# Performance work log

Measured on AMD Instinct MI355X. Metric: run time of the kernel, lower is better.

Reference implementation:

```python
import jax, jax.numpy as jnp
import numpy as np

N = 256
MAX_LENGTH = 1024
BATCH = 32768


def _transition(n):
    # HiPPO-LegS transition matrices (float64 numpy, matches torch module)
    q = np.arange(n, dtype=np.float64)
    col, row = np.meshgrid(q, q)
    r = 2 * q + 1
    M = -(np.where(row >= col, r, 0) - np.diag(q))
    T = np.sqrt(np.diag(2 * q + 1))
    A = T @ M @ np.linalg.inv(T)
    B = np.diag(T)  # squeezed (N,)
    return A, B


def _build_stacked(n, max_length):
    # Bilinear (Tustin) discretization at every timescale t=1..max_length.
    A, B = _transition(n)
    ts = np.arange(1, max_length + 1, dtype=np.float64)  # (L,)
    At = A[None] / ts[:, None, None]                     # (L,N,N)
    Bt = B[None] / ts[:, None]                           # (L,N)
    I = np.eye(n)
    lhs = I[None] - At / 2                               # (L,N,N), lower triangular
    A_stacked = np.linalg.solve(lhs, I[None] + At / 2)   # (L,N,N)
    B_stacked = np.linalg.solve(lhs, Bt[..., None])[..., 0]  # (L,N)
    return A_stacked.astype(np.float32), B_stacked.astype(np.float32)


def setup_inputs() -> dict:
    key = jax.random.key(0)
    k1, k2 = jax.random.split(key)
    A_np, B_np = _build_stacked(N, MAX_LENGTH)
    return {
        "c": jax.random.normal(k1, (BATCH, N), dtype=jnp.float32),
        "f": jax.random.normal(k2, (BATCH, 1), dtype=jnp.float32),
        "A_stacked": jnp.asarray(A_np),  # (L, N, N) buffer
        "B_stacked": jnp.asarray(B_np),  # (L, N) buffer
        "t": 512,
    }


def reference(c, f, A_stacked, B_stacked, t):
    # F.linear(c, A) == c @ A.T ; then scaled add of new value f
    A = A_stacked[t]            # (N, N)
    b = B_stacked[t]            # (N,)
    return c @ A.T + b * f      # (BATCH, N)
```

## Files before the change

### kernel.cpp

```cpp
#include <hip/hip_runtime.h>
#include <cstdint>
#include <cstddef>

typedef _Float16 half8 __attribute__((ext_vector_type(8)));
typedef float f32x4 __attribute__((ext_vector_type(4)));

static constexpr int kN  = 256;
static constexpr int kBM = 64;
static constexpr size_t kHalfB  = 64 * 1024;
static constexpr size_t kLDS    = kHalfB;

__global__ __launch_bounds__(256) void hippo_prep(
    const float* __restrict__ A_stacked, const int* __restrict__ tptr,
    _Float16* __restrict__ a16)
{
    const int t = tptr[0];
    const float* __restrict__ A = A_stacked + (size_t)t * kN * kN;
    const int tid = blockIdx.x * 256 + threadIdx.x;
    const int ksh = tid >> 12;
    const int nt  = (tid >> 8) & 15;
    const int ks2 = (tid >> 6) & 3;
    const int l   = tid & 63;
    const int row = nt * 16 + (l & 15);
    const int k0  = (ksh * 4 + ks2) * 32 + ((l >> 4) << 3);
    const float* __restrict__ src = A + (size_t)row * kN + k0;
    f32x4 v0 = *(const f32x4*)(src);
    f32x4 v1 = *(const f32x4*)(src + 4);
    half8 h;
    h[0] = (_Float16)v0[0]; h[1] = (_Float16)v0[1];
    h[2] = (_Float16)v0[2]; h[3] = (_Float16)v0[3];
    h[4] = (_Float16)v1[0]; h[5] = (_Float16)v1[1];
    h[6] = (_Float16)v1[2]; h[7] = (_Float16)v1[3];
    ((half8*)a16)[tid] = h;
}

__global__ __launch_bounds__(256, 2) void hippo_gemm(
    const float* __restrict__ c, const float* __restrict__ f,
    const float* __restrict__ Bst, const int* __restrict__ tptr,
    const _Float16* __restrict__ a16, float* __restrict__ out)
{
    extern __shared__ char lds_raw[];

    const int tid  = threadIdx.x;
    const int l    = tid & 63;
    const int wid  = tid >> 6;
    const int lo16 = l & 15;
    const int hi4  = l >> 4;
    const int bid  = blockIdx.x;
    const int m0   = bid * kBM + wid * 16;

    const char* __restrict__ gsrc1 = (const char*)a16 + kHalfB;
    #pragma unroll
    for (int j = 0; j < 4; ++j) {
        const int nt = wid + j * 4;
        const int kmax = (nt - 8) >> 1;
        for (int ks2 = 0; ks2 <= kmax && ks2 < 4; ++ks2) {
            const size_t off = (size_t)(nt * 4 + ks2) * 1024 + (size_t)l * 16;
            __builtin_amdgcn_global_load_lds(
                (const __attribute__((address_space(1))) void*)(gsrc1 + off),
                (__attribute__((address_space(3))) void*)(lds_raw + off),
                16, 0, 0);
        }
    }

    const float* __restrict__ cptr = c + (size_t)(m0 + lo16) * kN + (hi4 << 3);
    f32x4 cv0[4], cv1[4];
    #pragma unroll
    for (int ks = 0; ks < 4; ++ks) {
        cv0[ks] = *(const f32x4*)(cptr + 128 + ks * 32);
        cv1[ks] = *(const f32x4*)(cptr + 128 + ks * 32 + 4);
    }

    const int t = tptr[0];
    const float* __restrict__ brow = Bst + (size_t)t * kN;
    float bvs[16];
    #pragma unroll
    for (int nt = 0; nt < 16; ++nt) bvs[nt] = brow[nt * 16 + lo16];
    float fv[4];
    #pragma unroll
    for (int r = 0; r < 4; ++r) fv[r] = f[m0 + (hi4 << 2) + r];

    __syncthreads();

    half8 af[4];
    #pragma unroll
    for (int ks = 0; ks < 4; ++ks) {
        af[ks][0] = (_Float16)cv0[ks][0]; af[ks][1] = (_Float16)cv0[ks][1];
        af[ks][2] = (_Float16)cv0[ks][2]; af[ks][3] = (_Float16)cv0[ks][3];
        af[ks][4] = (_Float16)cv1[ks][0]; af[ks][5] = (_Float16)cv1[ks][1];
        af[ks][6] = (_Float16)cv1[ks][2]; af[ks][7] = (_Float16)cv1[ks][3];
    }

    f32x4 dv0[4], dv1[4];
    #pragma unroll
    for (int ks = 0; ks < 4; ++ks) {
        dv0[ks] = *(const f32x4*)(cptr + ks * 32);
        dv1[ks] = *(const f32x4*)(cptr + ks * 32 + 4);
    }

    const half8* __restrict__ Bs = (const half8*)lds_raw;
    f32x4 acc[16];
    #pragma unroll
    for (int i = 0; i < 16; ++i) acc[i] = (f32x4){0.f, 0.f, 0.f, 0.f};
    #pragma unroll
    for (int ks2 = 0; ks2 < 4; ++ks2) {
        #pragma unroll
        for (int nt = 0; nt < 16; ++nt) {
            if (nt >= 8 + 2 * ks2) {
                half8 bf = Bs[(nt * 4 + ks2) * 64 + l];
                acc[nt] = __builtin_amdgcn_mfma_f32_16x16x32_f16(af[ks2], bf, acc[nt], 0, 0, 0);
            }
        }
    }

    __syncthreads();

    const char* __restrict__ gsrc0 = (const char*)a16;
    #pragma unroll
    for (int j = 0; j < 4; ++j) {
        const int nt = wid + j * 4;
        const int kmax = nt >> 1;
        for (int ks2 = 0; ks2 <= kmax && ks2 < 4; ++ks2) {
            const size_t off = (size_t)(nt * 4 + ks2) * 1024 + (size_t)l * 16;
            __builtin_amdgcn_global_load_lds(
                (const __attribute__((address_space(1))) void*)(gsrc0 + off),
                (__attribute__((address_space(3))) void*)(lds_raw + off),
                16, 0, 0);
        }
    }
    half8 ag[4];
    #pragma unroll
    for (int ks = 0; ks < 4; ++ks) {
        ag[ks][0] = (_Float16)dv0[ks][0]; ag[ks][1] = (_Float16)dv0[ks][1];
        ag[ks][2] = (_Float16)dv0[ks][2]; ag[ks][3] = (_Float16)dv0[ks][3];
        ag[ks][4] = (_Float16)dv1[ks][0]; ag[ks][5] = (_Float16)dv1[ks][1];
        ag[ks][6] = (_Float16)dv1[ks][2]; ag[ks][7] = (_Float16)dv1[ks][3];
    }

    __syncthreads();

    float* __restrict__ obase = out + (size_t)(m0 + (hi4 << 2)) * kN + lo16;
    #pragma unroll
    for (int nt = 0; nt < 16; ++nt) {
        f32x4 a = acc[nt];
        #pragma unroll
        for (int ks2 = 0; ks2 < 4; ++ks2) {
            if (ks2 <= (nt >> 1)) {
                half8 bf = Bs[(nt * 4 + ks2) * 64 + l];
                a = __builtin_amdgcn_mfma_f32_16x16x32_f16(ag[ks2], bf, a, 0, 0, 0);
            }
        }
        #pragma unroll
        for (int r = 0; r < 4; ++r)
            obase[(size_t)r * kN + nt * 16] = a[r] + bvs[nt] * fv[r];
    }
}

extern "C" void kernel_launch(void* const* d_in, const int* in_sizes, int n_in,
                              void* d_out, int out_size, void* d_ws, size_t ws_size,
                              hipStream_t stream) {
    const float* c   = (const float*)d_in[0];
    const float* f   = (const float*)d_in[1];
    const float* A   = (const float*)d_in[2];
    const float* B   = (const float*)d_in[3];
    const int*   t   = (const int*)d_in[4];
    float* out = (float*)d_out;
    _Float16* a16 = (_Float16*)d_ws;

    const int batch = in_sizes[0] / kN;

    hipFuncSetAttribute((const void*)hippo_gemm,
                        hipFuncAttributeMaxDynamicSharedMemorySize,
                        (int)kLDS);

    hipLaunchKernelGGL(hippo_prep, dim3(32), dim3(256), 0, stream, A, t, a16);
    hipLaunchKernelGGL(hippo_gemm, dim3(batch / kBM), dim3(256), kLDS, stream,
                       c, f, B, t, a16, out);
}
```

Measured before the change: 22.08 us.

## Pack triangular A fragments into one LDS buffer and load once

Replaces the two-phase LDS staging of the fp16 A matrix (upper-k half, compute, sync, reload lower-k half, sync) with a single packed triangular layout. Only the nonzero fragments of the lower-triangular A are stored, addressed through a prefix-offset table, so everything fits in 72 KB of LDS. This removes two barriers and the reload stall between the halves. The cost is more LDS per block, which may lower occupancy below the two blocks per CU the launch bounds request, plus constant-memory table lookups in the address math.

Result: no change. 22.44 us (+1.6%).

```diff
diff --git a/kernel.cpp b/kernel.cpp
--- a/kernel.cpp
+++ b/kernel.cpp
@@ -7,8 +7,10 @@
 
 static constexpr int kN  = 256;
 static constexpr int kBM = 64;
-static constexpr size_t kHalfB  = 64 * 1024;
-static constexpr size_t kLDS    = kHalfB;
+static constexpr size_t kLDS = 72 * 1024;
+
+__device__ __constant__ const int kBase[16] =
+    {0, 1, 2, 4, 6, 9, 12, 16, 20, 25, 30, 36, 42, 49, 56, 64};
 
 __global__ __launch_bounds__(256) void hippo_prep(
     const float* __restrict__ A_stacked, const int* __restrict__ tptr,
@@ -49,17 +51,22 @@
     const int bid  = blockIdx.x;
     const int m0   = bid * kBM + wid * 16;
 
-    const char* __restrict__ gsrc1 = (const char*)a16 + kHalfB;
+    const char* __restrict__ gsrc = (const char*)a16;
     #pragma unroll
     for (int j = 0; j < 4; ++j) {
-        const int nt = wid + j * 4;
-        const int kmax = (nt - 8) >> 1;
-        for (int ks2 = 0; ks2 <= kmax && ks2 < 4; ++ks2) {
-            const size_t off = (size_t)(nt * 4 + ks2) * 1024 + (size_t)l * 16;
-            __builtin_amdgcn_global_load_lds(
-                (const __attribute__((address_space(1))) void*)(gsrc1 + off),
-                (__attribute__((address_space(3))) void*)(lds_raw + off),
-                16, 0, 0);
+        const int nt   = wid + j * 4;
+        const int kmax = nt >> 1;
+        #pragma unroll
+        for (int ks = 0; ks < 8; ++ks) {
+            if (ks <= kmax) {
+                const size_t soff =
+                    (size_t)(((ks >> 2) * 16 + nt) * 4 + (ks & 3)) * 1024 + (size_t)l * 16;
+                const size_t doff = (size_t)(kBase[nt] + ks) * 1024 + (size_t)l * 16;
+                __builtin_amdgcn_global_load_lds(
+                    (const __attribute__((address_space(1))) void*)(gsrc + soff),
+                    (__attribute__((address_space(3))) void*)(lds_raw + doff),
+                    16, 0, 0);
+            }
         }
     }
 
@@ -107,27 +114,12 @@
         #pragma unroll
         for (int nt = 0; nt < 16; ++nt) {
             if (nt >= 8 + 2 * ks2) {
-                half8 bf = Bs[(nt * 4 + ks2) * 64 + l];
+                half8 bf = Bs[(kBase[nt] + 4 + ks2) * 64 + l];
                 acc[nt] = __builtin_amdgcn_mfma_f32_16x16x32_f16(af[ks2], bf, acc[nt], 0, 0, 0);
             }
         }
     }
 
-    __syncthreads();
-
-    const char* __restrict__ gsrc0 = (const char*)a16;
-    #pragma unroll
-    for (int j = 0; j < 4; ++j) {
-        const int nt = wid + j * 4;
-        const int kmax = nt >> 1;
-        for (int ks2 = 0; ks2 <= kmax && ks2 < 4; ++ks2) {
-            const size_t off = (size_t)(nt * 4 + ks2) * 1024 + (size_t)l * 16;
-            __builtin_amdgcn_global_load_lds(
-                (const __attribute__((address_space(1))) void*)(gsrc0 + off),
-                (__attribute__((address_space(3))) void*)(lds_raw + off),
-                16, 0, 0);
-        }
-    }
     half8 ag[4];
     #pragma unroll
     for (int ks = 0; ks < 4; ++ks) {
@@ -137,8 +129,6 @@
         ag[ks][6] = (_Float16)dv1[ks][2]; ag[ks][7] = (_Float16)dv1[ks][3];
     }
 
-    __syncthreads();
-
     float* __restrict__ obase = out + (size_t)(m0 + (hi4 << 2)) * kN + lo16;
     #pragma unroll
     for (int nt = 0; nt < 16; ++nt) {
@@ -146,7 +136,7 @@
         #pragma unroll
         for (int ks2 = 0; ks2 < 4; ++ks2) {
             if (ks2 <= (nt >> 1)) {
-                half8 bf = Bs[(nt * 4 + ks2) * 64 + l];
+                half8 bf = Bs[(kBase[nt] + ks2) * 64 + l];
                 a = __builtin_amdgcn_mfma_f32_16x16x32_f16(ag[ks2], bf, a, 0, 0, 0);
             }
         }
```
